# Kernel optimization log

Hardware: AMD Instinct MI355X
Metric: run time of the kernel (lower is better)

## Reference

```python
import jax, jax.numpy as jnp
import numpy as np


def setup_inputs() -> dict:
    key = jax.random.key(0)
    kq, kk, kv = jax.random.split(key, 3)
    B, H, S, D = 2, 16, 2048, 64
    Q = jax.random.normal(kq, (B, H, S, D), dtype=jnp.float32)
    K = jax.random.normal(kk, (B, H, S, D), dtype=jnp.float32)
    V = jax.random.normal(kv, (B, H, S, D), dtype=jnp.float32)
    return {"Q": Q, "K": K, "V": V}


def reference(Q, K, V):
    # Faithful to the torch module: NO 1/sqrt(d_k) scaling (d_k is computed
    # but never used in the original forward).
    scores = jnp.einsum('bhqd,bhkd->bhqk', Q, K)      # [B,H,S,S]
    attn = jax.nn.softmax(scores, axis=-1)
    out = jnp.einsum('bhqk,bhkd->bhqd', attn, V)      # [B,H,S,D]
    return out
```

## Files before the change

### kernel.cpp

```cpp
#include <hip/hip_runtime.h>


typedef __bf16    bf16_t;
typedef _Float16  f16_t;
typedef __bf16    bf16x8 __attribute__((ext_vector_type(8)));
typedef _Float16  f16x8  __attribute__((ext_vector_type(8)));
typedef float     f32x4  __attribute__((ext_vector_type(4)));

constexpr int S  = 2048;
constexpr int Dh = 64;
constexpr int KT = 64;
constexpr int QT = 128;

__device__ __forceinline__ int sw(int row, int col) {
    return row * 64 + ((((col >> 3) ^ (row & 7)) << 3) | (col & 7));
}

template<bool SPLIT>
__global__ __launch_bounds__(256, 4)
void attn_kernel(const float* __restrict__ Qg,
                 const float* __restrict__ Kg,
                 const float* __restrict__ Vg,
                 float* __restrict__ Og,
                 float* __restrict__ Opart,
                 float* __restrict__ lpart)
{
    __shared__ f16_t  Khs[KT * Dh];
    __shared__ bf16_t Vts[Dh * KT];
    __shared__ bf16_t Pbs[QT * Dh];

    const int tid  = threadIdx.x;
    const int lane = tid & 63;
    const int wv   = tid >> 6;
    const int l15  = lane & 15;
    const int qd   = lane >> 4;
    const int wb   = wv * 32;

    const int bx   = blockIdx.x;
    const int head = bx & 31;
    const int r5   = bx >> 5;
    const int qt   = SPLIT ? (r5 >> 1) : r5;
    const int half = SPLIT ? (r5 & 1) : 0;
    const int tile = head * 16 + qt;
    const int ch0  = SPLIT ? half * 16 : 0;
    const int nch  = SPLIT ? 16 : 32;

    const float* Qp = Qg + (size_t)tile * QT * Dh;
    const float* Kp = Kg + (size_t)head * S * Dh;
    const float* Vp = Vg + (size_t)head * S * Dh;

    const int skey = tid >> 4;
    const int sc4  = (tid & 15) * 4;
    const int vkb  = (tid >> 4) * 4;
    const int vc4  = (tid & 15) * 4;

    f16x8 qf[2][2];
    #pragma unroll
    for (int sub = 0; sub < 2; ++sub) {
        const float* qrow = Qp + (size_t)(wb + sub * 16 + l15) * Dh;
        #pragma unroll
        for (int ks = 0; ks < 2; ++ks) {
            const float* p = qrow + ks * 32 + qd * 8;
            const float4 a = *(const float4*)(p);
            const float4 b = *(const float4*)(p + 4);
            const float xs[8] = {a.x, a.y, a.z, a.w, b.x, b.y, b.z, b.w};
            #pragma unroll
            for (int j = 0; j < 8; ++j) qf[sub][ks][j] = (f16_t)xs[j];
        }
    }

    f32x4 oa[2][4];
    float lp[2];
    #pragma unroll
    for (int s2 = 0; s2 < 2; ++s2) {
        lp[s2] = 0.f;
        #pragma unroll
        for (int t = 0; t < 4; ++t) oa[s2][t] = (f32x4){0.f, 0.f, 0.f, 0.f};
    }

    float4 kbuf[4], vbuf[4];
    {
        const float* Kc = Kp + (size_t)ch0 * KT * Dh;
        const float* Vc = Vp + (size_t)ch0 * KT * Dh;
        #pragma unroll
        for (int it = 0; it < 4; ++it)
            kbuf[it] = *(const float4*)(Kc + (size_t)(it * 16 + skey) * Dh + sc4);
        #pragma unroll
        for (int i = 0; i < 4; ++i)
            vbuf[i] = *(const float4*)(Vc + (size_t)(vkb + i) * Dh + vc4);
    }

    #pragma unroll 1
    for (int ci = 0; ci < nch; ++ci) {
        __syncthreads();

        #pragma unroll
        for (int it = 0; it < 4; ++it) {
            const float xs[4] = {kbuf[it].x, kbuf[it].y, kbuf[it].z, kbuf[it].w};
            union { f16_t h[4]; uint2 u; } ph;
            #pragma unroll
            for (int j = 0; j < 4; ++j) ph.h[j] = (f16_t)xs[j];
            *(uint2*)&Khs[sw(it * 16 + skey, sc4)] = ph.u;
        }
        {
            const float rs[4][4] = {{vbuf[0].x, vbuf[1].x, vbuf[2].x, vbuf[3].x},
                                    {vbuf[0].y, vbuf[1].y, vbuf[2].y, vbuf[3].y},
                                    {vbuf[0].z, vbuf[1].z, vbuf[2].z, vbuf[3].z},
                                    {vbuf[0].w, vbuf[1].w, vbuf[2].w, vbuf[3].w}};
            #pragma unroll
            for (int i = 0; i < 4; ++i) {
                union { bf16_t h[4]; uint2 u; } pv;
                #pragma unroll
                for (int j = 0; j < 4; ++j) pv.h[j] = (bf16_t)rs[i][j];
                *(uint2*)&Vts[sw(vc4 + i, vkb)] = pv.u;
            }
        }
        __syncthreads();

        if (ci + 1 < nch) {
            const float* Kc = Kp + (size_t)(ch0 + ci + 1) * KT * Dh;
            const float* Vc = Vp + (size_t)(ch0 + ci + 1) * KT * Dh;
            #pragma unroll
            for (int it = 0; it < 4; ++it)
                kbuf[it] = *(const float4*)(Kc + (size_t)(it * 16 + skey) * Dh + sc4);
            #pragma unroll
            for (int i = 0; i < 4; ++i)
                vbuf[i] = *(const float4*)(Vc + (size_t)(vkb + i) * Dh + vc4);
        }

        #pragma unroll
        for (int np = 0; np < 2; ++np) {
            f32x4 st[2][2];
            #pragma unroll
            for (int s2 = 0; s2 < 2; ++s2)
                #pragma unroll
                for (int t = 0; t < 2; ++t) st[s2][t] = (f32x4){0.f, 0.f, 0.f, 0.f};
            #pragma unroll
            for (int ks = 0; ks < 2; ++ks) {
                const int co = ks * 32 + qd * 8;
                const f16x8 ak0 = *(const f16x8*)&Khs[sw((np * 2 + 0) * 16 + l15, co)];
                const f16x8 ak1 = *(const f16x8*)&Khs[sw((np * 2 + 1) * 16 + l15, co)];
                #pragma unroll
                for (int s2 = 0; s2 < 2; ++s2) {
                    st[s2][0] = __builtin_amdgcn_mfma_f32_16x16x32_f16(ak0, qf[s2][ks], st[s2][0], 0, 0, 0);
                    st[s2][1] = __builtin_amdgcn_mfma_f32_16x16x32_f16(ak1, qf[s2][ks], st[s2][1], 0, 0, 0);
                }
            }
            #pragma unroll
            for (int s2 = 0; s2 < 2; ++s2) {
                #pragma unroll
                for (int t = 0; t < 2; ++t) {
                    union { bf16_t h[4]; uint2 u; } pb;
                    #pragma unroll
                    for (int r = 0; r < 4; ++r) {
                        const bf16_t b = (bf16_t)__expf(st[s2][t][r]);
                        lp[s2] += (float)b;
                        pb.h[r] = b;
                    }
                    *(uint2*)&Pbs[sw(wb + s2 * 16 + l15, (np * 2 + t) * 16 + qd * 4)] = pb.u;
                }
            }
        }

        #pragma unroll
        for (int ks = 0; ks < 2; ++ks) {
            const int co = ks * 32 + qd * 8;
            const bf16x8 pa0 = *(const bf16x8*)&Pbs[sw(wb + l15,      co)];
            const bf16x8 pa1 = *(const bf16x8*)&Pbs[sw(wb + 16 + l15, co)];
            #pragma unroll
            for (int dt = 0; dt < 4; ++dt) {
                const bf16x8 vb = *(const bf16x8*)&Vts[sw(dt * 16 + l15, co)];
                oa[0][dt] = __builtin_amdgcn_mfma_f32_16x16x32_bf16(pa0, vb, oa[0][dt], 0, 0, 0);
                oa[1][dt] = __builtin_amdgcn_mfma_f32_16x16x32_bf16(pa1, vb, oa[1][dt], 0, 0, 0);
            }
        }
    }

    #pragma unroll
    for (int s2 = 0; s2 < 2; ++s2) {
        lp[s2] += __shfl_xor(lp[s2], 16, 64);
        lp[s2] += __shfl_xor(lp[s2], 32, 64);
    }

    if (SPLIT) {
        float* Po = Opart + (size_t)(tile * 2 + half) * (QT * Dh);
        float* lq = lpart + (size_t)(tile * 2 + half) * QT;
        #pragma unroll
        for (int s2 = 0; s2 < 2; ++s2) {
            if (qd == 0) lq[wb + s2 * 16 + l15] = lp[s2];
            #pragma unroll
            for (int r = 0; r < 4; ++r) {
                const int row = wb + s2 * 16 + qd * 4 + r;
                #pragma unroll
                for (int dt = 0; dt < 4; ++dt)
                    Po[(size_t)row * Dh + dt * 16 + l15] = oa[s2][dt][r];
            }
        }
    } else {
        float* Op = Og + (size_t)tile * QT * Dh;
        #pragma unroll
        for (int s2 = 0; s2 < 2; ++s2) {
            #pragma unroll
            for (int r = 0; r < 4; ++r) {
                const float inv = 1.0f / __shfl(lp[s2], qd * 4 + r, 64);
                const int row = wb + s2 * 16 + qd * 4 + r;
                #pragma unroll
                for (int dt = 0; dt < 4; ++dt)
                    Op[(size_t)row * Dh + dt * 16 + l15] = oa[s2][dt][r] * inv;
            }
        }
    }
}

__global__ __launch_bounds__(256)
void combine_kernel(const float* __restrict__ Opart,
                    const float* __restrict__ lpart,
                    float* __restrict__ Og)
{
    const int i  = blockIdx.x * 256 + threadIdx.x;
    const int q  = i >> 11;
    const int rw = (i >> 4) & 127;
    const size_t e = (size_t)(i & 2047) * 4;
    const float4 a = *(const float4*)(Opart + (size_t)(2 * q)     * (QT * Dh) + e);
    const float4 b = *(const float4*)(Opart + (size_t)(2 * q + 1) * (QT * Dh) + e);
    const float  l = lpart[(size_t)(2 * q) * QT + rw] + lpart[(size_t)(2 * q + 1) * QT + rw];
    const float inv = 1.0f / l;
    float4 o;
    o.x = (a.x + b.x) * inv;
    o.y = (a.y + b.y) * inv;
    o.z = (a.z + b.z) * inv;
    o.w = (a.w + b.w) * inv;
    *(float4*)(Og + (size_t)i * 4) = o;
}

extern "C" void kernel_launch(void* const* d_in, const int* in_sizes, int n_in,
                              void* d_out, int out_size, void* d_ws, size_t ws_size,
                              hipStream_t stream)
{
    const float* Q = (const float*)d_in[0];
    const float* K = (const float*)d_in[1];
    const float* V = (const float*)d_in[2];
    float*       O = (float*)d_out;

    constexpr size_t NPART       = 1024;
    constexpr size_t OPART_ELEMS = NPART * QT * Dh;
    constexpr size_t LPART_ELEMS = NPART * QT;
    constexpr size_t NEED = (OPART_ELEMS + LPART_ELEMS) * sizeof(float);

    if (ws_size >= NEED) {
        float* Opart = (float*)d_ws;
        float* lpart = Opart + OPART_ELEMS;
        attn_kernel<true><<<dim3(1024), dim3(256), 0, stream>>>(
            Q, K, V, nullptr, Opart, lpart);
        const int n4 = (int)(OPART_ELEMS / 2 / 4);
        combine_kernel<<<dim3(n4 / 256), dim3(256), 0, stream>>>(Opart, lpart, O);
    } else {
        attn_kernel<false><<<dim3(512), dim3(256), 0, stream>>>(
            Q, K, V, O, nullptr, nullptr);
    }
}
```

Before: 153.5 us.

## Double-buffer K/V LDS tiles and interleave P·V per half-chunk

K and V shared-memory tiles are double-buffered so the next chunk is converted and staged while the current one is consumed, which removes one of the two block barriers per iteration and issues global prefetch two chunks ahead. The P staging buffer is halved and the P·V MFMAs are moved inside the key-half loop, so each 32-key slice of probabilities is consumed right after it is produced. This adds LDS use for K/V but shrinks P, and may change occupancy and register pressure. P is written and read by the same wave without a barrier, which relies on wave-local ordering.

```diff
diff --git a/kernel.cpp b/kernel.cpp
--- a/kernel.cpp
+++ b/kernel.cpp
@@ -14,6 +14,9 @@
 
 __device__ __forceinline__ int sw(int row, int col) {
     return row * 64 + ((((col >> 3) ^ (row & 7)) << 3) | (col & 7));
+}
+__device__ __forceinline__ int swp(int row, int col) {
+    return row * 32 + ((((col >> 3) ^ (row & 3)) << 3) | (col & 7));
 }
 
 template<bool SPLIT>
@@ -25,9 +28,9 @@
                  float* __restrict__ Opart,
                  float* __restrict__ lpart)
 {
-    __shared__ f16_t  Khs[KT * Dh];
-    __shared__ bf16_t Vts[Dh * KT];
-    __shared__ bf16_t Pbs[QT * Dh];
+    __shared__ f16_t  Khs[2][KT * Dh];
+    __shared__ bf16_t Vts[2][Dh * KT];
+    __shared__ bf16_t Pbs[QT * 32];
 
     const int tid  = threadIdx.x;
     const int lane = tid & 63;
@@ -79,54 +82,51 @@
     }
 
     float4 kbuf[4], vbuf[4];
-    {
-        const float* Kc = Kp + (size_t)ch0 * KT * Dh;
-        const float* Vc = Vp + (size_t)ch0 * KT * Dh;
+
+    auto load_chunk = [&](int ch) {
+        const float* Kc = Kp + (size_t)ch * KT * Dh;
+        const float* Vc = Vp + (size_t)ch * KT * Dh;
         #pragma unroll
         for (int it = 0; it < 4; ++it)
             kbuf[it] = *(const float4*)(Kc + (size_t)(it * 16 + skey) * Dh + sc4);
         #pragma unroll
         for (int i = 0; i < 4; ++i)
             vbuf[i] = *(const float4*)(Vc + (size_t)(vkb + i) * Dh + vc4);
-    }
+    };
+    auto stage = [&](int b) {
+        #pragma unroll
+        for (int it = 0; it < 4; ++it) {
+            const float xs[4] = {kbuf[it].x, kbuf[it].y, kbuf[it].z, kbuf[it].w};
+            union { f16_t h[4]; uint2 u; } ph;
+            #pragma unroll
+            for (int j = 0; j < 4; ++j) ph.h[j] = (f16_t)xs[j];
+            *(uint2*)&Khs[b][sw(it * 16 + skey, sc4)] = ph.u;
+        }
+        const float rs[4][4] = {{vbuf[0].x, vbuf[1].x, vbuf[2].x, vbuf[3].x},
+                                {vbuf[0].y, vbuf[1].y, vbuf[2].y, vbuf[3].y},
+                                {vbuf[0].z, vbuf[1].z, vbuf[2].z, vbuf[3].z},
+                                {vbuf[0].w, vbuf[1].w, vbuf[2].w, vbuf[3].w}};
+        #pragma unroll
+        for (int i = 0; i < 4; ++i) {
+            union { bf16_t h[4]; uint2 u; } pv;
+            #pragma unroll
+            for (int j = 0; j < 4; ++j) pv.h[j] = (bf16_t)rs[i][j];
+            *(uint2*)&Vts[b][sw(vc4 + i, vkb)] = pv.u;
+        }
+    };
+
+    load_chunk(ch0);
+    stage(0);
+    if (nch > 1) load_chunk(ch0 + 1);
 
     #pragma unroll 1
     for (int ci = 0; ci < nch; ++ci) {
         __syncthreads();
 
-        #pragma unroll
-        for (int it = 0; it < 4; ++it) {
-            const float xs[4] = {kbuf[it].x, kbuf[it].y, kbuf[it].z, kbuf[it].w};
-            union { f16_t h[4]; uint2 u; } ph;
-            #pragma unroll
-            for (int j = 0; j < 4; ++j) ph.h[j] = (f16_t)xs[j];
-            *(uint2*)&Khs[sw(it * 16 + skey, sc4)] = ph.u;
-        }
-        {
-            const float rs[4][4] = {{vbuf[0].x, vbuf[1].x, vbuf[2].x, vbuf[3].x},
-                                    {vbuf[0].y, vbuf[1].y, vbuf[2].y, vbuf[3].y},
-                                    {vbuf[0].z, vbuf[1].z, vbuf[2].z, vbuf[3].z},
-                                    {vbuf[0].w, vbuf[1].w, vbuf[2].w, vbuf[3].w}};
-            #pragma unroll
-            for (int i = 0; i < 4; ++i) {
-                union { bf16_t h[4]; uint2 u; } pv;
-                #pragma unroll
-                for (int j = 0; j < 4; ++j) pv.h[j] = (bf16_t)rs[i][j];
-                *(uint2*)&Vts[sw(vc4 + i, vkb)] = pv.u;
-            }
-        }
-        __syncthreads();
-
-        if (ci + 1 < nch) {
-            const float* Kc = Kp + (size_t)(ch0 + ci + 1) * KT * Dh;
-            const float* Vc = Vp + (size_t)(ch0 + ci + 1) * KT * Dh;
-            #pragma unroll
-            for (int it = 0; it < 4; ++it)
-                kbuf[it] = *(const float4*)(Kc + (size_t)(it * 16 + skey) * Dh + sc4);
-            #pragma unroll
-            for (int i = 0; i < 4; ++i)
-                vbuf[i] = *(const float4*)(Vc + (size_t)(vkb + i) * Dh + vc4);
-        }
+        if (ci + 1 < nch) stage((ci + 1) & 1);
+        if (ci + 2 < nch) load_chunk(ch0 + ci + 2);
+
+        const int cb = ci & 1;
 
         #pragma unroll
         for (int np = 0; np < 2; ++np) {
@@ -138,8 +138,8 @@
             #pragma unroll
             for (int ks = 0; ks < 2; ++ks) {
                 const int co = ks * 32 + qd * 8;
-                const f16x8 ak0 = *(const f16x8*)&Khs[sw((np * 2 + 0) * 16 + l15, co)];
-                const f16x8 ak1 = *(const f16x8*)&Khs[sw((np * 2 + 1) * 16 + l15, co)];
+                const f16x8 ak0 = *(const f16x8*)&Khs[cb][sw((np * 2 + 0) * 16 + l15, co)];
+                const f16x8 ak1 = *(const f16x8*)&Khs[cb][sw((np * 2 + 1) * 16 + l15, co)];
                 #pragma unroll
                 for (int s2 = 0; s2 < 2; ++s2) {
                     st[s2][0] = __builtin_amdgcn_mfma_f32_16x16x32_f16(ak0, qf[s2][ks], st[s2][0], 0, 0, 0);
@@ -157,19 +157,16 @@
                         lp[s2] += (float)b;
                         pb.h[r] = b;
                     }
-                    *(uint2*)&Pbs[sw(wb + s2 * 16 + l15, (np * 2 + t) * 16 + qd * 4)] = pb.u;
+                    *(uint2*)&Pbs[swp(wb + s2 * 16 + l15, t * 16 + qd * 4)] = pb.u;
                 }
             }
-        }
-
-        #pragma unroll
-        for (int ks = 0; ks < 2; ++ks) {
-            const int co = ks * 32 + qd * 8;
-            const bf16x8 pa0 = *(const bf16x8*)&Pbs[sw(wb + l15,      co)];
-            const bf16x8 pa1 = *(const bf16x8*)&Pbs[sw(wb + 16 + l15, co)];
+            const int cov = np * 32 + qd * 8;
+            const int cop = qd * 8;
+            const bf16x8 pa0 = *(const bf16x8*)&Pbs[swp(wb + l15,      cop)];
+            const bf16x8 pa1 = *(const bf16x8*)&Pbs[swp(wb + 16 + l15, cop)];
             #pragma unroll
             for (int dt = 0; dt < 4; ++dt) {
-                const bf16x8 vb = *(const bf16x8*)&Vts[sw(dt * 16 + l15, co)];
+                const bf16x8 vb = *(const bf16x8*)&Vts[cb][sw(dt * 16 + l15, cov)];
                 oa[0][dt] = __builtin_amdgcn_mfma_f32_16x16x32_bf16(pa0, vb, oa[0][dt], 0, 0, 0);
                 oa[1][dt] = __builtin_amdgcn_mfma_f32_16x16x32_bf16(pa1, vb, oa[1][dt], 0, 0, 0);
             }
```

Result: no change. 156.4 us (+1.9%).
